# Optimization experiments

Measured on AMD Instinct MI355X. Metric: run time of the kernel, lower is better.

The kernel has to match this reference:

```python
import jax, jax.numpy as jnp
import numpy as np

HIDDEN = 4096
N_HEADS = 32
N_KV_HEADS = 8
HEAD_DIM = 128
ROPE_THETA = 1000000.0
EPS = 1e-06
B, T = 1, 2048


def apply_rope(inputs, position_ids, head_dim, theta):
    # inputs: [B, T, H, D], position_ids: [B, T]
    fraction = 2 * jnp.arange(0, head_dim // 2, dtype=jnp.float32) / head_dim
    timescale = jnp.power(theta, fraction)  # [D/2]
    x = (position_ids.astype(jnp.float32)[..., None] / timescale[None, None, :])[..., None, :]  # [B,T,1,D/2]
    sin, cos = jnp.sin(x), jnp.cos(x)
    a, b = jnp.split(inputs, 2, axis=-1)
    return jnp.concatenate([a * cos - b * sin, b * cos + a * sin], axis=-1).astype(inputs.dtype)


def rms_norm(x, weight, eps=EPS):
    rms = jnp.sqrt(jnp.mean(x * x, axis=-1, keepdims=True) + eps)
    return weight * x / rms


def setup_inputs() -> dict:
    key = jax.random.key(0)
    ks = jax.random.split(key, 8)
    lecun = lambda k, shape: jax.random.normal(k, shape, jnp.float32) / np.sqrt(shape[0])
    return {
        "x": jax.random.normal(ks[0], (B, T, HIDDEN), jnp.float32),
        "Wq": lecun(ks[1], (HIDDEN, N_HEADS * HEAD_DIM)),
        "Wk": lecun(ks[2], (HIDDEN, N_KV_HEADS * HEAD_DIM)),
        "Wv": lecun(ks[3], (HIDDEN, N_KV_HEADS * HEAD_DIM)),
        "Wo": lecun(ks[4], (N_HEADS * HEAD_DIM, HIDDEN)),
        "q_norm_w": 1.0 + 0.01 * jax.random.normal(ks[5], (HEAD_DIM,), jnp.float32),
        "k_norm_w": 1.0 + 0.01 * jax.random.normal(ks[6], (HEAD_DIM,), jnp.float32),
        "attention_mask": jnp.ones((B, T), jnp.int32),
        "positions": jnp.broadcast_to(jnp.arange(T, dtype=jnp.int32)[None, :], (B, T)),
    }


def reference(x, Wq, Wk, Wv, Wo, q_norm_w, k_norm_w, attention_mask, positions):
    b, t, _ = x.shape
    q = rms_norm((x @ Wq).reshape(b, t, N_HEADS, HEAD_DIM), q_norm_w)
    k = rms_norm((x @ Wk).reshape(b, t, N_KV_HEADS, HEAD_DIM), k_norm_w)
    v = (x @ Wv).reshape(b, t, N_KV_HEADS, HEAD_DIM)
    q = apply_rope(q, positions, HEAD_DIM, ROPE_THETA)
    k = apply_rope(k, positions, HEAD_DIM, ROPE_THETA)
    # prefill path: kv_cache is None -> causal attention, padding mask on keys
    attn = jax.nn.dot_product_attention(
        q, k, v,
        scale=1.0 / HEAD_DIM ** 0.5,
        mask=attention_mask[:, None, None, :].astype(bool),
        is_causal=True,
    )
    out = attn.reshape(b, t, N_HEADS * HEAD_DIM) @ Wo
    return out, (k, v)
```

## Files before the change

### kernel.cpp

```cpp
#include <hip/hip_runtime.h>


typedef __bf16 bf16;
typedef __bf16 bf16x8 __attribute__((ext_vector_type(8)));
typedef float  f32x4  __attribute__((ext_vector_type(4)));

#define MFMA16(a, b, c) __builtin_amdgcn_mfma_f32_16x16x32_bf16((a), (b), (c), 0, 0, 0)

__global__ __launch_bounds__(256) void detect_convert(
    const unsigned short* __restrict__ probe,
    const void* __restrict__ qw_raw, const void* __restrict__ kw_raw,
    int* __restrict__ flag, bf16* __restrict__ qwc, bf16* __restrict__ kwc) {
    __shared__ int cnt;
    if (threadIdx.x == 0) cnt = 0;
    __syncthreads();
    int local = 0;
    for (int i = 0; i < 4; ++i) {
        const unsigned short w = probe[(threadIdx.x * 4 + i) * 2];
        const int e = (w >> 7) & 0xFF;
        if (e >= 90 && e <= 140) ++local;
    }
    atomicAdd(&cnt, local);
    __syncthreads();
    const bool isbf16 = cnt >= 700;
    if (threadIdx.x == 0) *flag = isbf16 ? 1 : 0;
    const int t = threadIdx.x;
    if (t < 128)
        qwc[t] = isbf16 ? ((const bf16*)qw_raw)[t] : (bf16)((const float*)qw_raw)[t];
    else
        kwc[t - 128] = isbf16 ? ((const bf16*)kw_raw)[t - 128] : (bf16)((const float*)kw_raw)[t - 128];
}

__global__ __launch_bounds__(256) void convert_x(const void* __restrict__ xv,
                                                 bf16* __restrict__ xb,
                                                 const int* __restrict__ flag) {
    const size_t i8 = ((size_t)blockIdx.x * 256 + threadIdx.x) * 8;
    if (*flag) {
        *(bf16x8*)&xb[i8] = *(const bf16x8*)&((const bf16*)xv)[i8];
    } else {
        const f32x4 a = *(const f32x4*)&((const float*)xv)[i8];
        const f32x4 b = *(const f32x4*)&((const float*)xv)[i8 + 4];
        bf16x8 o;
#pragma unroll
        for (int e = 0; e < 4; ++e) { o[e] = (bf16)a[e]; o[e + 4] = (bf16)b[e]; }
        *(bf16x8*)&xb[i8] = o;
    }
}

#define GBM 128
#define GBN 128
#define GBK 64
#define GLD 72

__global__ __launch_bounds__(256) void gemm_nt(
    const bf16* __restrict__ A,
    const void* __restrict__ B1v, const void* __restrict__ B2v, const void* __restrict__ B3v,
    bf16* __restrict__ Cb1, float* __restrict__ Cf1,
    bf16* __restrict__ Cb2, float* __restrict__ Cf2,
    bf16* __restrict__ Cb3, float* __restrict__ Cf3,
    const int* __restrict__ flag, int K,
    int ldb1, int ldb2, int ldb3, int ldc1, int ldc2, int ldc3,
    int ns1, int ns2) {
    __shared__ __align__(16) bf16 As[2][GBM * GLD];
    __shared__ __align__(16) bf16 Bs[2][GBN * GLD];

    const int nbxp = (int)gridDim.x >> 3;
    int id = blockIdx.y * gridDim.x + blockIdx.x;
    const int xcd = id & 7;
    const int j = id >> 3;
    const int bx = xcd * nbxp + j / (int)gridDim.y;
    const int by = j % (int)gridDim.y;

    const void* Bv;
    bf16* Cb;
    float* Cf;
    int n0, ldb, ldc;
    if (bx < ns1) {
        Bv = B1v; Cb = Cb1; Cf = Cf1; n0 = bx * GBN; ldb = ldb1; ldc = ldc1;
    } else if (bx < ns1 + ns2) {
        Bv = B2v; Cb = Cb2; Cf = Cf2; n0 = (bx - ns1) * GBN; ldb = ldb2; ldc = ldc2;
    } else {
        Bv = B3v; Cb = Cb3; Cf = Cf3; n0 = (bx - ns1 - ns2) * GBN; ldb = ldb3; ldc = ldc3;
    }
    const int m0 = by * GBM;

    const bool bBf16 = (*flag) != 0;
    const bf16*  Bb = (const bf16*)Bv;
    const float* Bf = (const float*)Bv;

    const int tid  = threadIdx.x;
    const int wave = tid >> 6;
    const int lane = tid & 63;
    const int l15  = lane & 15;
    const int quad = lane >> 4;
    const int wm = (wave >> 1) * 64;
    const int wn = (wave & 1) * 64;

    const int ar[4] = { (0 * 256 + tid) >> 3, (1 * 256 + tid) >> 3,
                        (2 * 256 + tid) >> 3, (3 * 256 + tid) >> 3 };
    const int ak = tid & 7;

    f32x4 acc[4][4];
#pragma unroll
    for (int i = 0; i < 4; ++i)
#pragma unroll
        for (int j2 = 0; j2 < 4; ++j2) acc[i][j2] = {0.f, 0.f, 0.f, 0.f};

    bf16x8 aReg[4];
    bf16   bReg[4][8];

#define LOAD_TILE(k0)                                                          \
    {                                                                          \
        _Pragma("unroll")                                                      \
        for (int p = 0; p < 4; ++p)                                            \
            aReg[p] = *(const bf16x8*)&A[(size_t)(m0 + ar[p]) * K + (k0) + ak * 8]; \
        if (bBf16) {                                                           \
            _Pragma("unroll")                                                  \
            for (int p = 0; p < 4; ++p) {                                      \
                const int w16 = wave * 4 + p;                                  \
                const int n = (w16 & 1) * 64 + lane, kc = w16 >> 1;            \
                _Pragma("unroll")                                              \
                for (int e = 0; e < 8; ++e)                                    \
                    bReg[p][e] = Bb[(size_t)((k0) + kc * 8 + e) * ldb + n0 + n]; \
            }                                                                  \
        } else {                                                               \
            _Pragma("unroll")                                                  \
            for (int p = 0; p < 4; ++p) {                                      \
                const int w16 = wave * 4 + p;                                  \
                const int n = (w16 & 1) * 64 + lane, kc = w16 >> 1;            \
                _Pragma("unroll")                                              \
                for (int e = 0; e < 8; ++e)                                    \
                    bReg[p][e] = (bf16)Bf[(size_t)((k0) + kc * 8 + e) * ldb + n0 + n]; \
            }                                                                  \
        }                                                                      \
    }

#define WRITE_TILE(buf)                                                        \
    {                                                                          \
        _Pragma("unroll")                                                      \
        for (int p = 0; p < 4; ++p)                                            \
            *(bf16x8*)&As[buf][ar[p] * GLD + ak * 8] = aReg[p];                \
        _Pragma("unroll")                                                      \
        for (int p = 0; p < 4; ++p) {                                          \
            const int w16 = wave * 4 + p;                                      \
            const int n = (w16 & 1) * 64 + lane, kc = w16 >> 1;                \
            bf16x8 bv;                                                         \
            _Pragma("unroll")                                                  \
            for (int e = 0; e < 8; ++e) bv[e] = bReg[p][e];                    \
            *(bf16x8*)&Bs[buf][n * GLD + kc * 8] = bv;                         \
        }                                                                      \
    }

#define COMPUTE_TILE(buf)                                                      \
    {                                                                          \
        _Pragma("unroll")                                                      \
        for (int kk = 0; kk < GBK; kk += 32) {                                 \
            bf16x8 af[4], bfr[4];                                              \
            _Pragma("unroll")                                                  \
            for (int i = 0; i < 4; ++i)                                        \
                af[i] = *(const bf16x8*)&As[buf][(wm + i * 16 + l15) * GLD + kk + quad * 8]; \
            _Pragma("unroll")                                                  \
            for (int j3 = 0; j3 < 4; ++j3)                                     \
                bfr[j3] = *(const bf16x8*)&Bs[buf][(wn + j3 * 16 + l15) * GLD + kk + quad * 8]; \
            _Pragma("unroll")                                                  \
            for (int i = 0; i < 4; ++i)                                        \
                _Pragma("unroll")                                              \
                for (int j3 = 0; j3 < 4; ++j3)                                 \
                    acc[i][j3] = MFMA16(af[i], bfr[j3], acc[i][j3]);           \
        }                                                                      \
    }

    const int nt = K >> 6;
    LOAD_TILE(0);
    WRITE_TILE(0);
    __syncthreads();
    int cur = 0;
    for (int t = 0; t < nt; ++t) {
        if (t + 1 < nt) LOAD_TILE((t + 1) << 6);
        COMPUTE_TILE(cur);
        if (t + 1 < nt) {
            WRITE_TILE(cur ^ 1);
            __syncthreads();
        }
        cur ^= 1;
    }
#undef LOAD_TILE
#undef WRITE_TILE
#undef COMPUTE_TILE

#pragma unroll
    for (int i = 0; i < 4; ++i)
#pragma unroll
        for (int j2 = 0; j2 < 4; ++j2)
#pragma unroll
            for (int r = 0; r < 4; ++r) {
                const int row = m0 + wm + i * 16 + quad * 4 + r;
                const int col = n0 + wn + j2 * 16 + l15;
                const float v = acc[i][j2][r];
                if (Cb) Cb[(size_t)row * ldc + col] = (bf16)v;
                if (Cf) Cf[(size_t)row * ldc + col] = v;
            }
}

__global__ __launch_bounds__(256) void norm_rope(const bf16* __restrict__ src,
                                                 bf16* __restrict__ dst_bf,
                                                 float* __restrict__ dst_f32,
                                                 const bf16* __restrict__ w,
                                                 const int* __restrict__ positions,
                                                 int H) {
    const int wid  = blockIdx.x * 4 + (threadIdx.x >> 6);
    const int lane = threadIdx.x & 63;
    const int token = wid / H, head = wid % H;
    const bf16* s = src + ((size_t)token * H + head) * 128;
    const float f0 = (float)s[lane], f1 = (float)s[lane + 64];
    float ss = f0 * f0 + f1 * f1;
    for (int off = 32; off >= 1; off >>= 1) ss += __shfl_xor(ss, off);
    const float inv_rms = rsqrtf(ss * (1.0f / 128.0f) + 1e-6f);
    const float n0 = f0 * inv_rms * (float)w[lane];
    const float n1 = f1 * inv_rms * (float)w[lane + 64];
    const float pos = (float)positions[token];
    const float inv_ts = expf((float)lane * (-13.815510557964274f / 64.0f));
    const float ang = pos * inv_ts;
    const float sn = sinf(ang), cs = cosf(ang);
    const float o0 = n0 * cs - n1 * sn;
    const float o1 = n1 * cs + n0 * sn;
    const size_t base = ((size_t)token * H + head) * 128;
    if (dst_bf)  { dst_bf[base + lane] = (bf16)o0;  dst_bf[base + lane + 64] = (bf16)o1; }
    if (dst_f32) { dst_f32[base + lane] = o0;       dst_f32[base + lane + 64] = o1; }
}

__global__ __launch_bounds__(256) void flash_attn(const bf16* __restrict__ Q,
                                                  const bf16* __restrict__ Kg,
                                                  const bf16* __restrict__ Vg,
                                                  bf16* __restrict__ Og) {
    __shared__ __align__(16) bf16 Ks[32 * 128];
    __shared__ __align__(16) bf16 Vt[128 * 40];
    __shared__ __align__(16) bf16 Ps[4][16 * 40];

    int id = blockIdx.y * 32 + blockIdx.x;
    id = (id & 7) * 128 + (id >> 3);
    const int h  = id >> 5;
    const int qt = 31 - (id & 31);
    const int kvh  = h >> 2;
    const int tid  = threadIdx.x;
    const int wave = tid >> 6;
    const int lane = tid & 63;
    const int l15  = lane & 15;
    const int quad = lane >> 4;
    const int q0   = qt * 64;
    const int qw0  = q0 + wave * 16;
    const int myq  = qw0 + l15;
    const float scale = 0.08838834764831845f;

    bf16x8 qf[4];
    {
        const bf16* qrow = Q + ((size_t)myq * 32 + h) * 128;
#pragma unroll
        for (int kc = 0; kc < 4; ++kc)
            qf[kc] = *(const bf16x8*)&qrow[kc * 32 + quad * 8];
    }

    f32x4 oacc[8];
#pragma unroll
    for (int i = 0; i < 8; ++i) oacc[i] = {0.f, 0.f, 0.f, 0.f};
    float m_run = -1e30f, l_run = 0.f;

    const int ksr  = tid & 31;
    const int kscb = tid >> 5;
    const int vr0  = (tid & 15) * 2;
    const int vcb  = tid >> 4;

    char* kbytes = (char*)Ks;
    char* vbytes = (char*)Vt;
    char* pbytes = (char*)&Ps[wave][0];

    const int ntiles = (q0 + 64) >> 5;
    for (int kt = 0; kt < ntiles; ++kt) {
        const int kb = kt * 32;
        {
            const bf16* src = Kg + ((size_t)(kb + ksr) * 8 + kvh) * 128;
            const bf16x8 v0 = *(const bf16x8*)&src[kscb * 8];
            const bf16x8 v1 = *(const bf16x8*)&src[(kscb + 8) * 8];
            const int b0 = (ksr * 256 + kscb * 16) ^ ((ksr & 7) << 4);
            const int b1 = (ksr * 256 + (kscb + 8) * 16) ^ ((ksr & 7) << 4);
            *(bf16x8*)(kbytes + b0) = v0;
            *(bf16x8*)(kbytes + b1) = v1;
        }
        {
            const bf16* s0 = Vg + ((size_t)(kb + vr0) * 8 + kvh) * 128 + vcb * 8;
            const bf16x8 a = *(const bf16x8*)s0;
            const bf16x8 b = *(const bf16x8*)(s0 + 1024);
#pragma unroll
            for (int e = 0; e < 8; ++e) {
                union { bf16 hh[2]; unsigned int u; } pk;
                pk.hh[0] = a[e]; pk.hh[1] = b[e];
                *(unsigned int*)(vbytes + (vcb * 8 + e) * 80 + vr0 * 2) = pk.u;
            }
        }
        __syncthreads();

        f32x4 sacc[2];
        sacc[0] = {0.f, 0.f, 0.f, 0.f};
        sacc[1] = {0.f, 0.f, 0.f, 0.f};
#pragma unroll
        for (int st = 0; st < 2; ++st) {
            const int row = st * 16 + l15;
#pragma unroll
            for (int kc = 0; kc < 4; ++kc) {
                const int bofs = (row * 256 + kc * 64 + quad * 16) ^ ((row & 7) << 4);
                const bf16x8 kf = *(const bf16x8*)(kbytes + bofs);
                sacc[st] = MFMA16(kf, qf[kc], sacc[st]);
            }
        }

        float sv[8];
        float pm = -1e30f;
#pragma unroll
        for (int st = 0; st < 2; ++st)
#pragma unroll
            for (int r = 0; r < 4; ++r) {
                const int key = kb + st * 16 + quad * 4 + r;
                float s = sacc[st][r] * scale;
                if (key > myq) s = -1e30f;
                sv[st * 4 + r] = s;
                pm = fmaxf(pm, s);
            }
        pm = fmaxf(pm, __shfl_xor(pm, 16));
        pm = fmaxf(pm, __shfl_xor(pm, 32));
        const float m_new = fmaxf(m_run, pm);
        const float corr = __expf(m_run - m_new);
        float ps = 0.f;
        bf16 pb[8];
#pragma unroll
        for (int i = 0; i < 8; ++i) {
            const float p = __expf(sv[i] - m_new);
            ps += p;
            pb[i] = (bf16)p;
        }
        ps += __shfl_xor(ps, 16);
        ps += __shfl_xor(ps, 32);
        l_run = l_run * corr + ps;
        m_run = m_new;

#pragma unroll
        for (int st = 0; st < 2; ++st)
#pragma unroll
            for (int r = 0; r < 4; ++r)
                *(bf16*)(pbytes + l15 * 80 + (st * 16 + quad * 4 + r) * 2) = pb[st * 4 + r];

        float corrq[4];
#pragma unroll
        for (int r = 0; r < 4; ++r) corrq[r] = __shfl(corr, quad * 4 + r);
#pragma unroll
        for (int nt = 0; nt < 8; ++nt)
#pragma unroll
            for (int r = 0; r < 4; ++r) oacc[nt][r] *= corrq[r];

        const bf16x8 pf = *(const bf16x8*)(pbytes + l15 * 80 + quad * 16);
#pragma unroll
        for (int nt = 0; nt < 8; ++nt) {
            const bf16x8 vf = *(const bf16x8*)(vbytes + (nt * 16 + l15) * 80 + quad * 16);
            oacc[nt] = MFMA16(pf, vf, oacc[nt]);
        }
        __syncthreads();
    }

    const float rinv = 1.0f / l_run;
    float linv[4];
#pragma unroll
    for (int r = 0; r < 4; ++r) linv[r] = __shfl(rinv, quad * 4 + r);
#pragma unroll
    for (int nt = 0; nt < 8; ++nt)
#pragma unroll
        for (int r = 0; r < 4; ++r) {
            const int row = qw0 + quad * 4 + r;
            Og[((size_t)row * 32 + h) * 128 + nt * 16 + l15] = (bf16)(oacc[nt][r] * linv[r]);
        }
}

extern "C" void kernel_launch(void* const* d_in, const int* in_sizes, int n_in,
                              void* d_out, int out_size, void* d_ws, size_t ws_size,
                              hipStream_t stream) {
    const void* x  = d_in[0];
    const void* Wq = d_in[1];
    const void* Wk = d_in[2];
    const void* Wv = d_in[3];
    const void* Wo = d_in[4];
    const void* qw = d_in[5];
    const void* kw = d_in[6];
    const int* positions = (const int*)d_in[8];

    char* ws = (char*)d_ws;
    int*  flag    = (int*)ws;
    bf16* qwc     = (bf16*)(ws + 64);
    bf16* kwc     = (bf16*)(ws + 64 + 256);
    bf16* kq      = (bf16*)(ws + 4096);
    bf16* vb      = (bf16*)(ws + 4096 + 4194304);
    bf16* xb      = (bf16*)(ws + 4096 + 8388608);
    bf16* attnbuf = (bf16*)(ws + 4096 + 8388608);

    float* outf = (float*)d_out;
    float* Kof  = outf + 8388608;
    float* Vof  = outf + 10485760;
    bf16*  qb   = (bf16*)d_out;

    detect_convert<<<1, 256, 0, stream>>>((const unsigned short*)Wq, qw, kw, flag, qwc, kwc);
    convert_x<<<4096, 256, 0, stream>>>(x, xb, flag);

    gemm_nt<<<dim3(48, 16), 256, 0, stream>>>(
        xb, Wq, Wk, Wv,
        qb, nullptr, kq, nullptr, vb, Vof,
        flag, 4096,
        4096, 1024, 1024, 4096, 1024, 1024,
        32, 8);

    norm_rope<<<16384, 256, 0, stream>>>(qb, qb, nullptr, qwc, positions, 32);
    norm_rope<<<4096, 256, 0, stream>>>(kq, kq, Kof, kwc, positions, 8);

    flash_attn<<<dim3(32, 32), 256, 0, stream>>>(qb, kq, vb, attnbuf);

    gemm_nt<<<dim3(32, 16), 256, 0, stream>>>(
        attnbuf, Wo, Wo, Wo,
        nullptr, outf, nullptr, nullptr, nullptr, nullptr,
        flag, 4096,
        4096, 4096, 4096, 4096, 4096, 4096,
        32, 0);
}
```

Measured before the change: 712.3 us.

## Load GEMM A tiles directly into swizzled LDS via global_load_lds

The projection GEMM now streams A tiles straight from global memory into LDS with global_load_lds. An XOR swizzle on the unpadded 64-wide rows keeps MFMA fragment reads free of bank conflicts. B stays register-staged but drops to a single LDS buffer, which costs an extra barrier per K step. The norm/RoPE kernel switches to the fast __expf and __sincosf intrinsics, which risks accuracy for large rotary angles.

```diff
diff --git a/kernel.cpp b/kernel.cpp
--- a/kernel.cpp
+++ b/kernel.cpp
@@ -6,6 +6,13 @@
 typedef float  f32x4  __attribute__((ext_vector_type(4)));
 
 #define MFMA16(a, b, c) __builtin_amdgcn_mfma_f32_16x16x32_bf16((a), (b), (c), 0, 0, 0)
+
+__device__ __forceinline__ void gll16(const void* g, void* l) {
+    __builtin_amdgcn_global_load_lds(
+        (const __attribute__((address_space(1))) void*)g,
+        (__attribute__((address_space(3))) void*)l,
+        16, 0, 0);
+}
 
 __global__ __launch_bounds__(256) void detect_convert(
     const unsigned short* __restrict__ probe,
@@ -61,8 +68,8 @@
     const int* __restrict__ flag, int K,
     int ldb1, int ldb2, int ldb3, int ldc1, int ldc2, int ldc3,
     int ns1, int ns2) {
-    __shared__ __align__(16) bf16 As[2][GBM * GLD];
-    __shared__ __align__(16) bf16 Bs[2][GBN * GLD];
+    __shared__ __align__(16) bf16 As[2][GBM * 64];
+    __shared__ __align__(16) bf16 Bs[GBN * GLD];
 
     const int nbxp = (int)gridDim.x >> 3;
     int id = blockIdx.y * gridDim.x + blockIdx.x;
@@ -93,12 +100,12 @@
     const int lane = tid & 63;
     const int l15  = lane & 15;
     const int quad = lane >> 4;
+    const int axor = l15 & 7;
     const int wm = (wave >> 1) * 64;
     const int wn = (wave & 1) * 64;
 
-    const int ar[4] = { (0 * 256 + tid) >> 3, (1 * 256 + tid) >> 3,
-                        (2 * 256 + tid) >> 3, (3 * 256 + tid) >> 3 };
-    const int ak = tid & 7;
+    const int l8 = lane >> 3;
+    const bf16* aP = A + (size_t)(m0 + wave * 8 + l8) * K + (((lane & 7) ^ l8) << 3);
 
     f32x4 acc[4][4];
 #pragma unroll
@@ -106,14 +113,10 @@
 #pragma unroll
         for (int j2 = 0; j2 < 4; ++j2) acc[i][j2] = {0.f, 0.f, 0.f, 0.f};
 
-    bf16x8 aReg[4];
-    bf16   bReg[4][8];
-
-#define LOAD_TILE(k0)                                                          \
+    bf16 bReg[4][8];
+
+#define LOAD_B(k0)                                                             \
     {                                                                          \
-        _Pragma("unroll")                                                      \
-        for (int p = 0; p < 4; ++p)                                            \
-            aReg[p] = *(const bf16x8*)&A[(size_t)(m0 + ar[p]) * K + (k0) + ak * 8]; \
         if (bBf16) {                                                           \
             _Pragma("unroll")                                                  \
             for (int p = 0; p < 4; ++p) {                                      \
@@ -135,11 +138,16 @@
         }                                                                      \
     }
 
-#define WRITE_TILE(buf)                                                        \
+#define GLL_A(k0, buf)                                                         \
     {                                                                          \
         _Pragma("unroll")                                                      \
         for (int p = 0; p < 4; ++p)                                            \
-            *(bf16x8*)&As[buf][ar[p] * GLD + ak * 8] = aReg[p];                \
+            gll16(aP + (size_t)p * 32 * K + (k0),                              \
+                  &As[buf][p * 2048 + wave * 512]);                            \
+    }
+
+#define WRITE_B()                                                              \
+    {                                                                          \
         _Pragma("unroll")                                                      \
         for (int p = 0; p < 4; ++p) {                                          \
             const int w16 = wave * 4 + p;                                      \
@@ -147,21 +155,22 @@
             bf16x8 bv;                                                         \
             _Pragma("unroll")                                                  \
             for (int e = 0; e < 8; ++e) bv[e] = bReg[p][e];                    \
-            *(bf16x8*)&Bs[buf][n * GLD + kc * 8] = bv;                         \
+            *(bf16x8*)&Bs[n * GLD + kc * 8] = bv;                              \
         }                                                                      \
     }
 
-#define COMPUTE_TILE(buf)                                                      \
+#define COMPUTE(buf)                                                           \
     {                                                                          \
         _Pragma("unroll")                                                      \
         for (int kk = 0; kk < GBK; kk += 32) {                                 \
             bf16x8 af[4], bfr[4];                                              \
             _Pragma("unroll")                                                  \
             for (int i = 0; i < 4; ++i)                                        \
-                af[i] = *(const bf16x8*)&As[buf][(wm + i * 16 + l15) * GLD + kk + quad * 8]; \
+                af[i] = *(const bf16x8*)&As[buf][(wm + i * 16 + l15) * 64 +    \
+                        ((((kk) >> 3) + quad) ^ axor) * 8];                    \
             _Pragma("unroll")                                                  \
             for (int j3 = 0; j3 < 4; ++j3)                                     \
-                bfr[j3] = *(const bf16x8*)&Bs[buf][(wn + j3 * 16 + l15) * GLD + kk + quad * 8]; \
+                bfr[j3] = *(const bf16x8*)&Bs[(wn + j3 * 16 + l15) * GLD + kk + quad * 8]; \
             _Pragma("unroll")                                                  \
             for (int i = 0; i < 4; ++i)                                        \
                 _Pragma("unroll")                                              \
@@ -171,22 +180,28 @@
     }
 
     const int nt = K >> 6;
-    LOAD_TILE(0);
-    WRITE_TILE(0);
+    LOAD_B(0);
+    GLL_A(0, 0);
+    WRITE_B();
     __syncthreads();
     int cur = 0;
     for (int t = 0; t < nt; ++t) {
-        if (t + 1 < nt) LOAD_TILE((t + 1) << 6);
-        COMPUTE_TILE(cur);
         if (t + 1 < nt) {
-            WRITE_TILE(cur ^ 1);
+            LOAD_B((t + 1) << 6);
+            GLL_A((t + 1) << 6, cur ^ 1);
+        }
+        COMPUTE(cur);
+        __syncthreads();
+        if (t + 1 < nt) {
+            WRITE_B();
             __syncthreads();
         }
         cur ^= 1;
     }
-#undef LOAD_TILE
-#undef WRITE_TILE
-#undef COMPUTE_TILE
+#undef LOAD_B
+#undef GLL_A
+#undef WRITE_B
+#undef COMPUTE
 
 #pragma unroll
     for (int i = 0; i < 4; ++i)
@@ -219,9 +234,10 @@
     const float n0 = f0 * inv_rms * (float)w[lane];
     const float n1 = f1 * inv_rms * (float)w[lane + 64];
     const float pos = (float)positions[token];
-    const float inv_ts = expf((float)lane * (-13.815510557964274f / 64.0f));
+    const float inv_ts = __expf((float)lane * (-13.815510557964274f / 64.0f));
     const float ang = pos * inv_ts;
-    const float sn = sinf(ang), cs = cosf(ang);
+    float sn, cs;
+    __sincosf(ang, &sn, &cs);
     const float o0 = n0 * cs - n1 * sn;
     const float o1 = n1 * cs + n0 * sn;
     const size_t base = ((size_t)token * H + head) * 128;
```

After: 639.9 us. 1.11x faster.
